# Kernel tuning notes

Measured on AMD Instinct MI355X. Metric: run time of the kernel, lower is better.

Reference implementation:

```python
import jax, jax.numpy as jnp
import numpy as np

B, S, D, H = 2, 2048, 1024, 16
HD = D // H

def setup_inputs() -> dict:
    key = jax.random.key(0)
    k1, k2, k3, k4, k5 = jax.random.split(key, 5)
    X = jax.random.normal(k1, (B, S, D), dtype=jnp.float32)
    # nn.Linear(D, 3D): weight [3D, D], bias [3D]
    W_qkv = jax.random.normal(k2, (3 * D, D), dtype=jnp.float32) * (1.0 / np.sqrt(D))
    b_qkv = jax.random.normal(k3, (3 * D,), dtype=jnp.float32) * 0.02
    W_out = jax.random.normal(k4, (D, D), dtype=jnp.float32) * (1.0 / np.sqrt(D))
    b_out = jax.random.normal(k5, (D,), dtype=jnp.float32) * 0.02
    return {"X": X, "W_qkv": W_qkv, "b_qkv": b_qkv, "W_out": W_out, "b_out": b_out}

def reference(X, W_qkv, b_qkv, W_out, b_out):
    b, s, d = X.shape
    qkv = jnp.einsum('bsd,ed->bse', X, W_qkv) + b_qkv  # [B,S,3D]
    q, k, v = jnp.split(qkv, 3, axis=2)
    def heads(t):
        return t.reshape(b, s, H, HD).transpose(0, 2, 1, 3)  # [B,H,S,HD]
    q, k, v = heads(q), heads(k), heads(v)
    scores = jnp.einsum('bhqd,bhkd->bhqk', q, k) * (1.0 / np.sqrt(HD))
    causal = jnp.tril(jnp.ones((s, s), dtype=bool))
    scores = jnp.where(causal[None, None], scores, jnp.float32(-jnp.inf))
    probs = jax.nn.softmax(scores, axis=-1)
    attn = jnp.einsum('bhqk,bhkd->bhqd', probs, v)  # [B,H,S,HD]
    attn = attn.transpose(0, 2, 1, 3).reshape(b, s, d)
    out = jnp.einsum('bsd,ed->bse', attn, W_out) + b_out
    return out
```

## Files before the change

### kernel.cpp

```cpp
#include <hip/hip_runtime.h>


typedef _Float16 f16x8 __attribute__((ext_vector_type(8)));
typedef _Float16 f16x4 __attribute__((ext_vector_type(4)));
typedef float    f32x4 __attribute__((ext_vector_type(4)));
typedef unsigned short u16x8 __attribute__((ext_vector_type(8)));

__device__ __forceinline__ float bf16_bits_to_f32(unsigned short u) {
    union { unsigned int i; float f; } v; v.i = ((unsigned int)u) << 16; return v.f;
}
__device__ __forceinline__ unsigned short f32_to_bf16_bits(float f) {
    union { float f; unsigned int i; } v; v.f = f;
    unsigned int x = v.i;
    return (unsigned short)((x + 0x7fffu + ((x >> 16) & 1u)) >> 16);
}
__device__ __forceinline__ float fexp2(float x) {
#if __has_builtin(__builtin_amdgcn_exp2f)
    return __builtin_amdgcn_exp2f(x);
#else
    return exp2f(x);
#endif
}
__device__ __forceinline__ void gll16(const void* g, void* l) {
    __builtin_amdgcn_global_load_lds(
        (const __attribute__((address_space(1))) unsigned int*)g,
        (__attribute__((address_space(3))) unsigned int*)l, 16, 0, 0);
}

__global__ void detect_kernel(const unsigned short* __restrict__ X, unsigned int* __restrict__ flag) {
    __shared__ unsigned int smax;
    if (threadIdx.x == 0) smax = 0;
    __syncthreads();
    unsigned int mymax = 0;
    for (int i = threadIdx.x; i < 16384; i += 256) {
        unsigned int e = (X[i] >> 7) & 0xFFu;
        mymax = mymax > e ? mymax : e;
    }
    atomicMax(&smax, mymax);
    __syncthreads();
    if (threadIdx.x == 0) flag[0] = (smax >= 0x90u) ? 1u : 0u;
}

__global__ void __launch_bounds__(256) cvt2_kernel(const void* __restrict__ Wqkv, _Float16* __restrict__ wout,
                                                   const void* __restrict__ X, _Float16* __restrict__ xout,
                                                   const unsigned int* __restrict__ flag) {
    int b = blockIdx.x;
    const void* in; _Float16* out; size_t off;
    if (b < 1536) { in = Wqkv; out = wout; off = (size_t)b * 2048; }
    else          { in = X;    out = xout; off = (size_t)(b - 1536) * 2048; }
    size_t i = off + (size_t)threadIdx.x * 8;
    f16x8 c;
    if (flag[0]) {
        const float* p = (const float*)in + i;
        #pragma unroll
        for (int j = 0; j < 8; j++) c[j] = (_Float16)p[j];
    } else {
        u16x8 r = *(const u16x8*)((const unsigned short*)in + i);
        #pragma unroll
        for (int j = 0; j < 8; j++) c[j] = (_Float16)bf16_bits_to_f32(r[j]);
    }
    *(f16x8*)(out + i) = c;
}

__global__ void __launch_bounds__(256) cvtw_kernel(const void* __restrict__ in,
                                                   _Float16* __restrict__ out,
                                                   const unsigned int* __restrict__ flag) {
    size_t i = ((size_t)blockIdx.x * 256 + threadIdx.x) * 8;
    f16x8 c;
    if (flag[0]) {
        const float* p = (const float*)in + i;
        #pragma unroll
        for (int j = 0; j < 8; j++) c[j] = (_Float16)p[j];
    } else {
        u16x8 r = *(const u16x8*)((const unsigned short*)in + i);
        #pragma unroll
        for (int j = 0; j < 8; j++) c[j] = (_Float16)bf16_bits_to_f32(r[j]);
    }
    *(f16x8*)(out + i) = c;
}

__device__ __forceinline__ void stage_ht(const _Float16* __restrict__ G, int kt, int h,
                                         _Float16* tile, int wave, int lane)
{
    #pragma unroll
    for (int i = 0; i < 2; i++) {
        int seg = wave * 2 + i;
        int f = seg * 64 + lane;
        int row = h * 128 + (f >> 3);
        int qg = (f & 7) ^ (row & 7);
        gll16(G + (size_t)row * 1024 + kt * 64 + qg * 8,
              tile + (size_t)h * 8192 + (size_t)seg * 512);
    }
}

__global__ void __launch_bounds__(512, 2) qkv_gemm8(
    const _Float16* __restrict__ Af, const _Float16* __restrict__ Wf,
    const void* __restrict__ bias, const unsigned int* __restrict__ flag,
    _Float16* __restrict__ qws, _Float16* __restrict__ kws, _Float16* __restrict__ vtws)
{
    __shared__ _Float16 L[2][2][16384];
    const int tid  = threadIdx.x;
    const int lane = tid & 63, wave = tid >> 6;
    const int l15  = lane & 15, quad = lane >> 4;
    const int wm   = (wave >> 2) * 128, wn = (wave & 3) * 64;
    const int m0   = blockIdx.y * 256, n0 = blockIdx.x * 256;
    const _Float16* Ag = Af + (size_t)m0 * 1024;
    const _Float16* Bg = Wf + (size_t)n0 * 1024;

    f32x4 acc[8][4] = {};

    stage_ht(Ag, 0, 0, &L[0][0][0], wave, lane);
    stage_ht(Ag, 0, 1, &L[0][0][0], wave, lane);
    stage_ht(Bg, 0, 0, &L[0][1][0], wave, lane);
    stage_ht(Bg, 0, 1, &L[0][1][0], wave, lane);
    stage_ht(Bg, 1, 0, &L[1][1][0], wave, lane);
    stage_ht(Bg, 1, 1, &L[1][1][0], wave, lane);
    stage_ht(Ag, 1, 0, &L[1][0][0], wave, lane);
    asm volatile("s_waitcnt vmcnt(6)" ::: "memory");
    __builtin_amdgcn_s_barrier();

    constexpr int NT = 16;
    #pragma unroll 2
    for (int t = 0; t < NT; ++t) {
        const int cb = t & 1;
        const _Float16* At = &L[cb][0][0];
        const _Float16* Bt = &L[cb][1][0];
        f16x8 aF[4][2], bF[4][2];

        #pragma unroll
        for (int mt = 0; mt < 4; mt++) {
            int R = wm + mt * 16 + l15;
            #pragma unroll
            for (int ks = 0; ks < 2; ks++)
                aF[mt][ks] = *(const f16x8*)&At[R * 64 + (((ks * 4 + quad) ^ (R & 7)) << 3)];
        }
        #pragma unroll
        for (int nt = 0; nt < 4; nt++) {
            int R = wn + nt * 16 + l15;
            #pragma unroll
            for (int ks = 0; ks < 2; ks++)
                bF[nt][ks] = *(const f16x8*)&Bt[R * 64 + (((ks * 4 + quad) ^ (R & 7)) << 3)];
        }
        if (t + 1 < NT) stage_ht(Ag, t + 1, 1, &L[(t + 1) & 1][0][0], wave, lane);
        __builtin_amdgcn_s_barrier();
        __builtin_amdgcn_s_setprio(1);
        #pragma unroll
        for (int mt = 0; mt < 4; mt++)
            #pragma unroll
            for (int nt = 0; nt < 2; nt++)
                #pragma unroll
                for (int ks = 0; ks < 2; ks++)
                    acc[mt][nt] = __builtin_amdgcn_mfma_f32_16x16x32_f16(aF[mt][ks], bF[nt][ks], acc[mt][nt], 0, 0, 0);
        __builtin_amdgcn_s_setprio(0);
        __builtin_amdgcn_s_barrier();

        if (t + 2 < NT) stage_ht(Bg, t + 2, 0, &L[cb][1][0], wave, lane);
        __builtin_amdgcn_s_barrier();
        __builtin_amdgcn_s_setprio(1);
        #pragma unroll
        for (int mt = 0; mt < 4; mt++)
            #pragma unroll
            for (int nt = 0; nt < 2; nt++)
                #pragma unroll
                for (int ks = 0; ks < 2; ks++)
                    acc[mt][2 + nt] = __builtin_amdgcn_mfma_f32_16x16x32_f16(aF[mt][ks], bF[2 + nt][ks], acc[mt][2 + nt], 0, 0, 0);
        __builtin_amdgcn_s_setprio(0);
        __builtin_amdgcn_s_barrier();

        #pragma unroll
        for (int mt = 0; mt < 4; mt++) {
            int R = wm + 64 + mt * 16 + l15;
            #pragma unroll
            for (int ks = 0; ks < 2; ks++)
                aF[mt][ks] = *(const f16x8*)&At[R * 64 + (((ks * 4 + quad) ^ (R & 7)) << 3)];
        }
        if (t + 2 < NT) stage_ht(Bg, t + 2, 1, &L[cb][1][0], wave, lane);
        __builtin_amdgcn_s_barrier();
        __builtin_amdgcn_s_setprio(1);
        #pragma unroll
        for (int mt = 0; mt < 4; mt++)
            #pragma unroll
            for (int nt = 0; nt < 2; nt++)
                #pragma unroll
                for (int ks = 0; ks < 2; ks++)
                    acc[4 + mt][2 + nt] = __builtin_amdgcn_mfma_f32_16x16x32_f16(aF[mt][ks], bF[2 + nt][ks], acc[4 + mt][2 + nt], 0, 0, 0);
        __builtin_amdgcn_s_setprio(0);
        __builtin_amdgcn_s_barrier();

        if (t + 2 < NT) stage_ht(Ag, t + 2, 0, &L[cb][0][0], wave, lane);
        if (t < NT - 2)       { asm volatile("s_waitcnt vmcnt(6)" ::: "memory"); }
        else if (t == NT - 2) { asm volatile("s_waitcnt vmcnt(0)" ::: "memory"); }
        __builtin_amdgcn_s_barrier();
        __builtin_amdgcn_s_setprio(1);
        #pragma unroll
        for (int mt = 0; mt < 4; mt++)
            #pragma unroll
            for (int nt = 0; nt < 2; nt++)
                #pragma unroll
                for (int ks = 0; ks < 2; ks++)
                    acc[4 + mt][nt] = __builtin_amdgcn_mfma_f32_16x16x32_f16(aF[mt][ks], bF[nt][ks], acc[4 + mt][nt], 0, 0, 0);
        __builtin_amdgcn_s_setprio(0);
        __builtin_amdgcn_s_barrier();
    }

    const bool isf32 = (flag[0] != 0u);
    const float qsc = 0.18033688011112042591f;
    #pragma unroll
    for (int nt = 0; nt < 4; nt++) {
        int n = n0 + wn + nt * 16 + l15;
        float bval = isf32 ? ((const float*)bias)[n] : bf16_bits_to_f32(((const unsigned short*)bias)[n]);
        int tn = n >> 10, e = n & 1023;
        int h = e >> 6, hd = e & 63;
        #pragma unroll
        for (int mt = 0; mt < 8; mt++) {
            #pragma unroll
            for (int r = 0; r < 4; r++) {
                int m = m0 + wm + mt * 16 + quad * 4 + r;
                float val = acc[mt][nt][r] + bval;
                int b = m >> 11, s = m & 2047;
                int bh = b * 16 + h;
                if (tn == 0)      qws [((size_t)bh * 2048 + s) * 64 + hd] = (_Float16)(val * qsc);
                else if (tn == 1) kws [((size_t)bh * 2048 + s) * 64 + hd] = (_Float16)val;
                else              vtws[((size_t)bh * 64 + hd) * 2048 + s] = (_Float16)val;
            }
        }
    }
}

template<int AF16>
__global__ void __launch_bounds__(256) qkv_gemm(
    const void* __restrict__ A, const _Float16* __restrict__ Wf,
    const void* __restrict__ bias, const unsigned int* __restrict__ flag,
    _Float16* __restrict__ qws, _Float16* __restrict__ kws, _Float16* __restrict__ vtws)
{
    constexpr int AST = AF16 ? 32 : 56;
    __shared__ _Float16 As[128 * AST];
    __shared__ _Float16 Bs[128 * 32];
    const bool isf32 = (flag[0] != 0u);
    const int tid  = threadIdx.x;
    const int lane = tid & 63, wave = tid >> 6;
    const int l15  = lane & 15, quad = lane >> 4;
    const int wm   = (wave >> 1) * 64, wn = (wave & 1) * 64;
    const int m0   = blockIdx.y * 128, n0 = blockIdx.x * 128;
    const int srow = tid >> 1, scol = (tid & 1) * 16;

    f32x4 acc[4][4] = {};

    for (int k0 = 0; k0 < 1024; k0 += 32) {
        if (AF16) {
            #pragma unroll
            for (int i = 0; i < 2; i++) {
                int seg = (wave * 2 + i) * 64 + lane;
                int row = seg >> 2, qtr = seg & 3;
                gll16((const _Float16*)A + (size_t)(m0 + row) * 1024 + k0 + qtr * 8,
                      &As[(wave * 2 + i) * 512]);
            }
        } else {
            f16x8 c0, c1;
            if (isf32) {
                const float4* ga = (const float4*)((const float*)A + (size_t)(m0 + srow) * 1024 + k0 + scol);
                float4 a0 = ga[0], a1 = ga[1], a2 = ga[2], a3 = ga[3];
                c0[0]=(_Float16)a0.x; c0[1]=(_Float16)a0.y; c0[2]=(_Float16)a0.z; c0[3]=(_Float16)a0.w;
                c0[4]=(_Float16)a1.x; c0[5]=(_Float16)a1.y; c0[6]=(_Float16)a1.z; c0[7]=(_Float16)a1.w;
                c1[0]=(_Float16)a2.x; c1[1]=(_Float16)a2.y; c1[2]=(_Float16)a2.z; c1[3]=(_Float16)a2.w;
                c1[4]=(_Float16)a3.x; c1[5]=(_Float16)a3.y; c1[6]=(_Float16)a3.z; c1[7]=(_Float16)a3.w;
            } else {
                const unsigned short* ga = (const unsigned short*)A + (size_t)(m0 + srow) * 1024 + k0 + scol;
                u16x8 r0 = *(const u16x8*)ga, r1 = *(const u16x8*)(ga + 8);
                #pragma unroll
                for (int i = 0; i < 8; i++) {
                    c0[i] = (_Float16)bf16_bits_to_f32(r0[i]);
                    c1[i] = (_Float16)bf16_bits_to_f32(r1[i]);
                }
            }
            *(f16x8*)&As[srow * AST + scol]     = c0;
            *(f16x8*)&As[srow * AST + scol + 8] = c1;
        }
        #pragma unroll
        for (int i = 0; i < 2; i++) {
            int seg = (wave * 2 + i) * 64 + lane;
            int row = seg >> 2, qtr = seg & 3;
            gll16(Wf + (size_t)(n0 + row) * 1024 + k0 + qtr * 8, &Bs[(wave * 2 + i) * 512]);
        }
        __syncthreads();
        f16x8 af[4], bfg[4];
        #pragma unroll
        for (int mt = 0; mt < 4; mt++)
            af[mt] = *(const f16x8*)&As[(wm + mt * 16 + l15) * AST + quad * 8];
        #pragma unroll
        for (int nt = 0; nt < 4; nt++)
            bfg[nt] = *(const f16x8*)&Bs[(wn + nt * 16 + l15) * 32 + quad * 8];
        #pragma unroll
        for (int mt = 0; mt < 4; mt++)
            #pragma unroll
            for (int nt = 0; nt < 4; nt++)
                acc[mt][nt] = __builtin_amdgcn_mfma_f32_16x16x32_f16(af[mt], bfg[nt], acc[mt][nt], 0, 0, 0);
        __syncthreads();
    }

    const float qsc = 0.18033688011112042591f;
    #pragma unroll
    for (int mt = 0; mt < 4; mt++) {
        #pragma unroll
        for (int nt = 0; nt < 4; nt++) {
            #pragma unroll
            for (int r = 0; r < 4; r++) {
                int m = m0 + wm + mt * 16 + quad * 4 + r;
                int n = n0 + wn + nt * 16 + l15;
                float bval = isf32 ? ((const float*)bias)[n] : bf16_bits_to_f32(((const unsigned short*)bias)[n]);
                float val = acc[mt][nt][r] + bval;
                int b = m >> 11, s = m & 2047;
                int t = n >> 10, e = n & 1023;
                int h = e >> 6, hd = e & 63;
                int bh = b * 16 + h;
                if (t == 0)      qws[((size_t)bh * 2048 + s) * 64 + hd]  = (_Float16)(val * qsc);
                else if (t == 1) kws[((size_t)bh * 2048 + s) * 64 + hd]  = (_Float16)val;
                else             vtws[((size_t)bh * 64 + hd) * 2048 + s] = (_Float16)val;
            }
        }
    }
}

__global__ void __launch_bounds__(256) out_gemm(
    const _Float16* __restrict__ Alo, const _Float16* __restrict__ Ahi,
    const _Float16* __restrict__ Wf, const void* __restrict__ bias,
    const unsigned int* __restrict__ flag, void* __restrict__ outp, int m_base)
{
    __shared__ _Float16 As[128 * 32];
    __shared__ _Float16 Bs[128 * 32];
    const bool isf32 = (flag[0] != 0u);
    const int tid  = threadIdx.x;
    const int lane = tid & 63, wave = tid >> 6;
    const int l15  = lane & 15, quad = lane >> 4;
    const int wm   = (wave >> 1) * 64, wn = (wave & 1) * 64;
    const int m0g  = m_base + blockIdx.y * 128, n0 = blockIdx.x * 128;
    const _Float16* A = (m0g < 2048) ? (Alo + (size_t)m0g * 1024)
                                     : (Ahi + (size_t)(m0g - 2048) * 1024);
    f32x4 acc[4][4] = {};

    for (int k0 = 0; k0 < 1024; k0 += 32) {
        #pragma unroll
        for (int i = 0; i < 2; i++) {
            int seg = (wave * 2 + i) * 64 + lane;
            int row = seg >> 2, qtr = seg & 3;
            gll16(A + (size_t)row * 1024 + k0 + qtr * 8, &As[(wave * 2 + i) * 512]);
            gll16(Wf + (size_t)(n0 + row) * 1024 + k0 + qtr * 8, &Bs[(wave * 2 + i) * 512]);
        }
        __syncthreads();
        f16x8 af[4], bfg[4];
        #pragma unroll
        for (int mt = 0; mt < 4; mt++)
            af[mt] = *(const f16x8*)&As[(wm + mt * 16 + l15) * 32 + quad * 8];
        #pragma unroll
        for (int nt = 0; nt < 4; nt++)
            bfg[nt] = *(const f16x8*)&Bs[(wn + nt * 16 + l15) * 32 + quad * 8];
        #pragma unroll
        for (int mt = 0; mt < 4; mt++)
            #pragma unroll
            for (int nt = 0; nt < 4; nt++)
                acc[mt][nt] = __builtin_amdgcn_mfma_f32_16x16x32_f16(af[mt], bfg[nt], acc[mt][nt], 0, 0, 0);
        __syncthreads();
    }

    #pragma unroll
    for (int mt = 0; mt < 4; mt++) {
        #pragma unroll
        for (int nt = 0; nt < 4; nt++) {
            #pragma unroll
            for (int r = 0; r < 4; r++) {
                int m = m0g + wm + mt * 16 + quad * 4 + r;
                int n = n0 + wn + nt * 16 + l15;
                float bval = isf32 ? ((const float*)bias)[n] : bf16_bits_to_f32(((const unsigned short*)bias)[n]);
                float val = acc[mt][nt][r] + bval;
                size_t idx = (size_t)m * 1024 + n;
                if (isf32) ((float*)outp)[idx] = val;
                else       ((unsigned short*)outp)[idx] = f32_to_bf16_bits(val);
            }
        }
    }
}

__global__ void __launch_bounds__(256) flash_kernel(
    const _Float16* __restrict__ qws,
    const _Float16* __restrict__ kws,
    const _Float16* __restrict__ vtws,
    _Float16* __restrict__ attn_lo,
    _Float16* __restrict__ attn_hi)
{
    __shared__ _Float16 Ks[2][64 * 64];
    __shared__ _Float16 Vs[2][64 * 72];

    const int bh   = blockIdx.x;
    const int qb   = 31 - blockIdx.y;
    const int tid  = threadIdx.x;
    const int wave = tid >> 6;
    const int lane = tid & 63;
    const int l15  = lane & 15, quad = lane >> 4;

    const _Float16* Q  = qws  + (size_t)bh * 2048 * 64;
    const _Float16* Kp = kws  + (size_t)bh * 2048 * 64;
    const _Float16* Vt = vtws + (size_t)bh * 64 * 2048;

    const int q0w = qb * 64 + wave * 16;
    f16x8 qf0 = *(const f16x8*)(Q + (size_t)(q0w + l15) * 64 + quad * 8);
    f16x8 qf1 = *(const f16x8*)(Q + (size_t)(q0w + l15) * 64 + 32 + quad * 8);

    f32x4 o[4] = {};
    float lp = 0.f;
    const int nch = qb + 1;

    {
        #pragma unroll
        for (int i = 0; i < 2; i++) {
            int s = (wave * 2 + i) * 64 + lane;
            int row = s >> 3, cs = ((s & 7) - row) & 7;
            gll16(Kp + (size_t)row * 64 + cs * 8, &Ks[0][s * 8]);
        }
        int hd = tid >> 3, ko = (tid & 7) * 8;
        f16x8 v0 = *(const f16x8*)(Vt + (size_t)hd * 2048 + ko);
        f16x8 v1 = *(const f16x8*)(Vt + (size_t)(hd + 32) * 2048 + ko);
        *(f16x8*)&Vs[0][hd * 72 + ko]        = v0;
        *(f16x8*)&Vs[0][(hd + 32) * 72 + ko] = v1;
    }

    for (int c = 0; c < nch; c++) {
        __syncthreads();
        const int cb = c & 1;
        const bool more = (c + 1 < nch);
        f16x8 vr0, vr1;
        int hd = tid >> 3, ko = (tid & 7) * 8;
        if (more) {
            int jn = (c + 1) * 64;
            vr0 = *(const f16x8*)(Vt + (size_t)hd * 2048 + jn + ko);
            vr1 = *(const f16x8*)(Vt + (size_t)(hd + 32) * 2048 + jn + ko);
            #pragma unroll
            for (int i = 0; i < 2; i++) {
                int s = (wave * 2 + i) * 64 + lane;
                int row = s >> 3, cs = ((s & 7) - row) & 7;
                gll16(Kp + (size_t)(jn + row) * 64 + cs * 8, &Ks[cb ^ 1][s * 8]);
            }
        }

        const bool diag = (c == qb);
        f32x4 t[4];
        #pragma unroll
        for (int kt = 0; kt < 4; kt++) {
            int row = kt * 16 + l15;
            f16x8 k0 = *(const f16x8*)&Ks[cb][row * 64 + ((quad + l15) & 7) * 8];
            f16x8 k1 = *(const f16x8*)&Ks[cb][row * 64 + ((4 + quad + l15) & 7) * 8];
            f32x4 z = {};
            z = __builtin_amdgcn_mfma_f32_16x16x32_f16(k0, qf0, z, 0, 0, 0);
            t[kt] = __builtin_amdgcn_mfma_f32_16x16x32_f16(k1, qf1, z, 0, 0, 0);
        }
        float p[16];
        #pragma unroll
        for (int kt = 0; kt < 4; kt++)
            #pragma unroll
            for (int r = 0; r < 4; r++) {
                float v = t[kt][r];
                if (diag)
                    v = ((kt * 16 + quad * 4 + r) <= (wave * 16 + l15)) ? v : -INFINITY;
                p[kt * 4 + r] = fminf(fexp2(v), 60000.0f);
            }
        float rs = 0.f;
        #pragma unroll
        for (int i = 0; i < 16; i++) rs += p[i];
        lp += rs;
        f16x4 pf[4];
        #pragma unroll
        for (int kt = 0; kt < 4; kt++)
            #pragma unroll
            for (int r = 0; r < 4; r++) pf[kt][r] = (_Float16)p[kt * 4 + r];
        #pragma unroll
        for (int kt = 0; kt < 4; kt++) {
            #pragma unroll
            for (int mt = 0; mt < 4; mt++) {
                f16x4 cv = *(const f16x4*)&Vs[cb][(mt * 16 + l15) * 72 + kt * 16 + quad * 4];
                o[mt] = __builtin_amdgcn_mfma_f32_16x16x16f16(cv, pf[kt], o[mt], 0, 0, 0);
            }
        }

        if (more) {
            *(f16x8*)&Vs[cb ^ 1][hd * 72 + ko]        = vr0;
            *(f16x8*)&Vs[cb ^ 1][(hd + 32) * 72 + ko] = vr1;
        }
    }

    const int b = bh >> 4, h = bh & 15;
    _Float16* attn = (b == 0) ? attn_lo : attn_hi;
    {
        float rs = lp;
        rs += __shfl_xor(rs, 16);
        rs += __shfl_xor(rs, 32);
        const float inv = 1.0f / rs;
        const int s = q0w + l15;
        #pragma unroll
        for (int mt = 0; mt < 4; mt++) {
            #pragma unroll
            for (int r = 0; r < 4; r++) {
                int hdd = mt * 16 + quad * 4 + r;
                attn[(size_t)s * 1024 + h * 64 + hdd] = (_Float16)(o[mt][r] * inv);
            }
        }
    }
}

extern "C" void kernel_launch(void* const* d_in, const int* in_sizes, int n_in,
                              void* d_out, int out_size, void* d_ws, size_t ws_size,
                              hipStream_t stream) {
    (void)out_size;
    const void *X = nullptr, *Wqkv = nullptr, *bqkv = nullptr, *Wout = nullptr, *bout = nullptr;
    for (int i = 0; i < n_in; i++) {
        switch (in_sizes[i]) {
            case 4194304: X    = d_in[i]; break;
            case 3145728: Wqkv = d_in[i]; break;
            case 3072:    bqkv = d_in[i]; break;
            case 1048576: Wout = d_in[i]; break;
            case 1024:    bout = d_in[i]; break;
        }
    }
    char* ws = (char*)d_ws;
    const size_t MB = 1u << 20;
    unsigned int* flag = (unsigned int*)ws;
    char* base = ws + 256;

    detect_kernel<<<1, 256, 0, stream>>>((const unsigned short*)X, flag);

    if (ws_size >= (size_t)(385 * MB / 10)) {
        _Float16* wf16 = (_Float16*)(base);
        _Float16* xf16 = (_Float16*)(base + 6 * MB);
        _Float16* q    = (_Float16*)(base + 14 * MB);
        _Float16* k    = (_Float16*)(base + 22 * MB);
        _Float16* vt   = (_Float16*)(base + 30 * MB);
        cvt2_kernel<<<dim3(3584), 256, 0, stream>>>(Wqkv, wf16, X, xf16, flag);
        qkv_gemm8<<<dim3(12, 16), 512, 0, stream>>>(xf16, wf16, bqkv, flag, q, k, vt);
        cvtw_kernel<<<dim3(512), 256, 0, stream>>>(Wout, wf16, flag);
        _Float16* attn = xf16;
        flash_kernel<<<dim3(32, 32), 256, 0, stream>>>(q, k, vt, attn, attn + (size_t)2048 * 1024);
        out_gemm<<<dim3(8, 32), 256, 0, stream>>>(attn, attn + (size_t)2048 * 1024,
                                                  wf16, bout, flag, d_out, 0);
    } else {
        _Float16* wf16    = (_Float16*)(base);
        _Float16* attn_hi = (_Float16*)(base + 6 * MB);
        _Float16* q       = (_Float16*)(base + 10 * MB);
        _Float16* k       = (_Float16*)(base + 18 * MB);
        _Float16* vt      = (_Float16*)(base + 26 * MB);
        _Float16* attn_lo = (_Float16*)((char*)d_out + 8 * MB);
        cvtw_kernel<<<dim3(1536), 256, 0, stream>>>(Wqkv, wf16, flag);
        qkv_gemm<0><<<dim3(24, 32), 256, 0, stream>>>(X, wf16, bqkv, flag, q, k, vt);
        cvtw_kernel<<<dim3(512), 256, 0, stream>>>(Wout, wf16, flag);
        flash_kernel<<<dim3(32, 32), 256, 0, stream>>>(q, k, vt, attn_lo, attn_hi);
        out_gemm<<<dim3(8, 16), 256, 0, stream>>>(attn_lo, attn_hi, wf16, bout, flag, d_out, 0);
        out_gemm<<<dim3(8, 16), 256, 0, stream>>>(attn_lo, attn_hi, wf16, bout, flag, d_out, 2048);
    }
}
```

Before: 222.7 us.

## Restructure QKV GEMM LDS layout, staging order, B-fragment reloads and block swizzle

Reorganizes the LDS tile layout so each staged half-tile holds interleaved row groups matching the wave quadrants, reorders the global-to-LDS staging so each buffer is refilled as soon as its consumers finish, and reloads only two B fragments per phase to cut register pressure. It also adds explicit ds_read_b128 with lgkmcnt waits and sched barriers, and a workgroup index swizzle that groups blocks for better L2 reuse. The aim is better overlap of loads with MFMA and lower VGPR use, at the cost of more LDS reads and tighter hand scheduling that could stall.

```diff
diff --git a/kernel.cpp b/kernel.cpp
--- a/kernel.cpp
+++ b/kernel.cpp
@@ -25,6 +25,13 @@
     __builtin_amdgcn_global_load_lds(
         (const __attribute__((address_space(1))) unsigned int*)g,
         (__attribute__((address_space(3))) unsigned int*)l, 16, 0, 0);
+}
+__device__ __forceinline__ f16x8 ds128(const _Float16* p) {
+    f16x8 r;
+    const __attribute__((address_space(3))) _Float16* lp =
+        (const __attribute__((address_space(3))) _Float16*)p;
+    asm volatile("ds_read_b128 %0, %1" : "=v"(r) : "v"(lp));
+    return r;
 }
 
 __global__ void detect_kernel(const unsigned short* __restrict__ X, unsigned int* __restrict__ flag) {
@@ -79,6 +86,7 @@
     *(f16x8*)(out + i) = c;
 }
 
+template<int MODE>
 __device__ __forceinline__ void stage_ht(const _Float16* __restrict__ G, int kt, int h,
                                          _Float16* tile, int wave, int lane)
 {
@@ -86,11 +94,19 @@
     for (int i = 0; i < 2; i++) {
         int seg = wave * 2 + i;
         int f = seg * 64 + lane;
-        int row = h * 128 + (f >> 3);
-        int qg = (f & 7) ^ (row & 7);
-        gll16(G + (size_t)row * 1024 + kt * 64 + qg * 8,
+        int lr = f >> 3;
+        int gr = (MODE == 0) ? ((lr & 63) + ((lr >> 6) << 7) + h * 64)
+                             : ((lr & 31) + ((lr >> 5) << 6) + h * 32);
+        int qg = (f & 7) ^ (lr & 7);
+        gll16(G + (size_t)gr * 1024 + kt * 64 + qg * 8,
               tile + (size_t)h * 8192 + (size_t)seg * 512);
     }
+}
+__device__ __forceinline__ int aoff(int R, int c) {
+    return (((R >> 6) & 1) << 13) + (((R & 63) | ((R >> 7) << 6)) << 6) + ((c ^ (R & 7)) << 3);
+}
+__device__ __forceinline__ int boff(int R, int c) {
+    return (((R >> 5) & 1) << 13) + (((R & 31) | ((R >> 6) << 5)) << 6) + ((c ^ (R & 7)) << 3);
 }
 
 __global__ void __launch_bounds__(512, 2) qkv_gemm8(
@@ -103,46 +119,50 @@
     const int lane = tid & 63, wave = tid >> 6;
     const int l15  = lane & 15, quad = lane >> 4;
     const int wm   = (wave >> 2) * 128, wn = (wave & 3) * 64;
-    const int m0   = blockIdx.y * 256, n0 = blockIdx.x * 256;
+
+    int wg   = blockIdx.y * 12 + blockIdx.x;
+    int swz  = (wg & 7) * 24 + (wg >> 3);
+    const int m0 = (swz / 12) * 256, n0 = (swz % 12) * 256;
     const _Float16* Ag = Af + (size_t)m0 * 1024;
     const _Float16* Bg = Wf + (size_t)n0 * 1024;
 
     f32x4 acc[8][4] = {};
-
-    stage_ht(Ag, 0, 0, &L[0][0][0], wave, lane);
-    stage_ht(Ag, 0, 1, &L[0][0][0], wave, lane);
-    stage_ht(Bg, 0, 0, &L[0][1][0], wave, lane);
-    stage_ht(Bg, 0, 1, &L[0][1][0], wave, lane);
-    stage_ht(Bg, 1, 0, &L[1][1][0], wave, lane);
-    stage_ht(Bg, 1, 1, &L[1][1][0], wave, lane);
-    stage_ht(Ag, 1, 0, &L[1][0][0], wave, lane);
+    f16x8 a[4][2], b[2][2];
+
+    stage_ht<0>(Ag, 0, 0, &L[0][0][0], wave, lane);
+    stage_ht<1>(Bg, 0, 0, &L[0][1][0], wave, lane);
+    stage_ht<1>(Bg, 0, 1, &L[0][1][0], wave, lane);
+    stage_ht<0>(Ag, 0, 1, &L[0][0][0], wave, lane);
+    stage_ht<0>(Ag, 1, 0, &L[1][0][0], wave, lane);
+    stage_ht<1>(Bg, 1, 1, &L[1][1][0], wave, lane);
+    stage_ht<0>(Ag, 1, 1, &L[1][0][0], wave, lane);
     asm volatile("s_waitcnt vmcnt(6)" ::: "memory");
     __builtin_amdgcn_s_barrier();
 
     constexpr int NT = 16;
-    #pragma unroll 2
     for (int t = 0; t < NT; ++t) {
         const int cb = t & 1;
         const _Float16* At = &L[cb][0][0];
         const _Float16* Bt = &L[cb][1][0];
-        f16x8 aF[4][2], bF[4][2];
 
         #pragma unroll
         for (int mt = 0; mt < 4; mt++) {
             int R = wm + mt * 16 + l15;
             #pragma unroll
             for (int ks = 0; ks < 2; ks++)
-                aF[mt][ks] = *(const f16x8*)&At[R * 64 + (((ks * 4 + quad) ^ (R & 7)) << 3)];
-        }
-        #pragma unroll
-        for (int nt = 0; nt < 4; nt++) {
+                a[mt][ks] = ds128(&At[aoff(R, ks * 4 + quad)]);
+        }
+        #pragma unroll
+        for (int nt = 0; nt < 2; nt++) {
             int R = wn + nt * 16 + l15;
             #pragma unroll
             for (int ks = 0; ks < 2; ks++)
-                bF[nt][ks] = *(const f16x8*)&Bt[R * 64 + (((ks * 4 + quad) ^ (R & 7)) << 3)];
-        }
-        if (t + 1 < NT) stage_ht(Ag, t + 1, 1, &L[(t + 1) & 1][0][0], wave, lane);
-        __builtin_amdgcn_s_barrier();
+                b[nt][ks] = ds128(&Bt[boff(R, ks * 4 + quad)]);
+        }
+        if (t + 1 < NT) stage_ht<1>(Bg, t + 1, 0, &L[cb ^ 1][1][0], wave, lane);
+        __builtin_amdgcn_s_barrier();
+        asm volatile("s_waitcnt lgkmcnt(0)" ::: "memory");
+        __builtin_amdgcn_sched_barrier(0);
         __builtin_amdgcn_s_setprio(1);
         #pragma unroll
         for (int mt = 0; mt < 4; mt++)
@@ -150,12 +170,21 @@
             for (int nt = 0; nt < 2; nt++)
                 #pragma unroll
                 for (int ks = 0; ks < 2; ks++)
-                    acc[mt][nt] = __builtin_amdgcn_mfma_f32_16x16x32_f16(aF[mt][ks], bF[nt][ks], acc[mt][nt], 0, 0, 0);
+                    acc[mt][nt] = __builtin_amdgcn_mfma_f32_16x16x32_f16(a[mt][ks], b[nt][ks], acc[mt][nt], 0, 0, 0);
         __builtin_amdgcn_s_setprio(0);
         __builtin_amdgcn_s_barrier();
 
-        if (t + 2 < NT) stage_ht(Bg, t + 2, 0, &L[cb][1][0], wave, lane);
-        __builtin_amdgcn_s_barrier();
+        #pragma unroll
+        for (int nt = 0; nt < 2; nt++) {
+            int R = wn + 32 + nt * 16 + l15;
+            #pragma unroll
+            for (int ks = 0; ks < 2; ks++)
+                b[nt][ks] = ds128(&Bt[boff(R, ks * 4 + quad)]);
+        }
+        if (t + 2 < NT) stage_ht<0>(Ag, t + 2, 0, &L[cb][0][0], wave, lane);
+        __builtin_amdgcn_s_barrier();
+        asm volatile("s_waitcnt lgkmcnt(0)" ::: "memory");
+        __builtin_amdgcn_sched_barrier(0);
         __builtin_amdgcn_s_setprio(1);
         #pragma unroll
         for (int mt = 0; mt < 4; mt++)
@@ -163,7 +192,7 @@
             for (int nt = 0; nt < 2; nt++)
                 #pragma unroll
                 for (int ks = 0; ks < 2; ks++)
-                    acc[mt][2 + nt] = __builtin_amdgcn_mfma_f32_16x16x32_f16(aF[mt][ks], bF[2 + nt][ks], acc[mt][2 + nt], 0, 0, 0);
+                    acc[mt][2 + nt] = __builtin_amdgcn_mfma_f32_16x16x32_f16(a[mt][ks], b[nt][ks], acc[mt][2 + nt], 0, 0, 0);
         __builtin_amdgcn_s_setprio(0);
         __builtin_amdgcn_s_barrier();
 
@@ -172,10 +201,12 @@
             int R = wm + 64 + mt * 16 + l15;
             #pragma unroll
             for (int ks = 0; ks < 2; ks++)
-                aF[mt][ks] = *(const f16x8*)&At[R * 64 + (((ks * 4 + quad) ^ (R & 7)) << 3)];
-        }
-        if (t + 2 < NT) stage_ht(Bg, t + 2, 1, &L[cb][1][0], wave, lane);
-        __builtin_amdgcn_s_barrier();
+                a[mt][ks] = ds128(&At[aoff(R, ks * 4 + quad)]);
+        }
+        if (t + 2 < NT) stage_ht<1>(Bg, t + 2, 1, &L[cb][1][0], wave, lane);
+        __builtin_amdgcn_s_barrier();
+        asm volatile("s_waitcnt lgkmcnt(0)" ::: "memory");
+        __builtin_amdgcn_sched_barrier(0);
         __builtin_amdgcn_s_setprio(1);
         #pragma unroll
         for (int mt = 0; mt < 4; mt++)
@@ -183,14 +214,23 @@
             for (int nt = 0; nt < 2; nt++)
                 #pragma unroll
                 for (int ks = 0; ks < 2; ks++)
-                    acc[4 + mt][2 + nt] = __builtin_amdgcn_mfma_f32_16x16x32_f16(aF[mt][ks], bF[2 + nt][ks], acc[4 + mt][2 + nt], 0, 0, 0);
+                    acc[4 + mt][2 + nt] = __builtin_amdgcn_mfma_f32_16x16x32_f16(a[mt][ks], b[nt][ks], acc[4 + mt][2 + nt], 0, 0, 0);
         __builtin_amdgcn_s_setprio(0);
         __builtin_amdgcn_s_barrier();
 
-        if (t + 2 < NT) stage_ht(Ag, t + 2, 0, &L[cb][0][0], wave, lane);
+        #pragma unroll
+        for (int nt = 0; nt < 2; nt++) {
+            int R = wn + nt * 16 + l15;
+            #pragma unroll
+            for (int ks = 0; ks < 2; ks++)
+                b[nt][ks] = ds128(&Bt[boff(R, ks * 4 + quad)]);
+        }
+        if (t + 2 < NT) stage_ht<0>(Ag, t + 2, 1, &L[cb][0][0], wave, lane);
         if (t < NT - 2)       { asm volatile("s_waitcnt vmcnt(6)" ::: "memory"); }
         else if (t == NT - 2) { asm volatile("s_waitcnt vmcnt(0)" ::: "memory"); }
         __builtin_amdgcn_s_barrier();
+        asm volatile("s_waitcnt lgkmcnt(0)" ::: "memory");
+        __builtin_amdgcn_sched_barrier(0);
         __builtin_amdgcn_s_setprio(1);
         #pragma unroll
         for (int mt = 0; mt < 4; mt++)
@@ -198,7 +238,7 @@
             for (int nt = 0; nt < 2; nt++)
                 #pragma unroll
                 for (int ks = 0; ks < 2; ks++)
-                    acc[4 + mt][nt] = __builtin_amdgcn_mfma_f32_16x16x32_f16(aF[mt][ks], bF[nt][ks], acc[4 + mt][nt], 0, 0, 0);
+                    acc[4 + mt][nt] = __builtin_amdgcn_mfma_f32_16x16x32_f16(a[mt][ks], b[nt][ks], acc[4 + mt][nt], 0, 0, 0);
         __builtin_amdgcn_s_setprio(0);
         __builtin_amdgcn_s_barrier();
     }
@@ -217,8 +257,8 @@
             for (int r = 0; r < 4; r++) {
                 int m = m0 + wm + mt * 16 + quad * 4 + r;
                 float val = acc[mt][nt][r] + bval;
-                int b = m >> 11, s = m & 2047;
-                int bh = b * 16 + h;
+                int bb = m >> 11, s = m & 2047;
+                int bh = bb * 16 + h;
                 if (tn == 0)      qws [((size_t)bh * 2048 + s) * 64 + hd] = (_Float16)(val * qsc);
                 else if (tn == 1) kws [((size_t)bh * 2048 + s) * 64 + hd] = (_Float16)val;
                 else              vtws[((size_t)bh * 64 + hd) * 2048 + s] = (_Float16)val;
```

Measured after the change: 224.9 us. About the same (+1.0%).
